# Performance work log

Measured on AMD Instinct MI355X. Metric: run time of the kernel, lower is better.

The kernel has to match this reference:

```python
import jax, jax.numpy as jnp
import numpy as np

N_NODES = 50000
N_EDGES = 800000
D_IN = 64
D_OUT = 64


def setup_inputs() -> dict:
    key = jax.random.key(0)
    k1, k2, k3, k4 = jax.random.split(key, 4)
    x = jax.random.normal(k1, (N_NODES, D_IN), dtype=jnp.float32)
    edge_index = jax.random.randint(k2, (2, N_EDGES), 0, N_NODES, dtype=jnp.int64)
    # GCNConv params: glorot weight [in, out], zero bias [out]
    limit = np.sqrt(6.0 / (D_IN + D_OUT)).astype(np.float32)
    W = jax.random.uniform(k3, (D_IN, D_OUT), minval=-limit, maxval=limit, dtype=jnp.float32)
    b = jnp.zeros((D_OUT,), dtype=jnp.float32)
    return {"x": x, "edge_index": edge_index, "W": W, "b": b}


def reference(x, edge_index, W, b):
    # GCNConv forward: linear transform, add self-loops, symmetric normalization,
    # scatter-add aggregation, bias.
    N = x.shape[0]
    xw = x @ W  # [N, D_OUT]

    self_loops = jnp.arange(N, dtype=edge_index.dtype)
    src = jnp.concatenate([edge_index[0], self_loops])  # source / neighbor j
    dst = jnp.concatenate([edge_index[1], self_loops])  # target / center i

    ones = jnp.ones_like(dst, dtype=xw.dtype)
    deg = jax.ops.segment_sum(ones, dst, num_segments=N)  # in-degree incl. self-loop
    deg_inv_sqrt = jnp.where(deg > 0, jax.lax.rsqrt(deg), 0.0)
    norm = deg_inv_sqrt[src] * deg_inv_sqrt[dst]  # [E+N]

    msgs = xw[src] * norm[:, None]  # gather + scale, [E+N, D_OUT]
    out = jax.ops.segment_sum(msgs, dst, num_segments=N)  # scatter-add
    return out + b
```

## Files before the change

kernel.cpp:

```cpp
#include <hip/hip_runtime.h>

constexpr int N_NODES = 50000;
constexpr int N_EDGES = 800000;
constexpr int D = 64;
constexpr int CAP = 64;
constexpr int NODES_PER_XCD = N_NODES / 8;

constexpr int OFF_CUR = 0;
constexpr int OFF_BKT = 50016;
constexpr int OFF_XW  = 3250016;

__device__ __forceinline__ float lo_bf(unsigned int u) {
    union { unsigned int x; float f; } c; c.x = u << 16; return c.f;
}
__device__ __forceinline__ float hi_bf(unsigned int u) {
    union { unsigned int x; float f; } c; c.x = u & 0xFFFF0000u; return c.f;
}
__device__ __forceinline__ unsigned short f2bf(float f) {
    union { float f; unsigned int u; } c; c.f = f;
    unsigned int r = (c.u + 0x7FFFu + ((c.u >> 16) & 1u)) >> 16;
    return (unsigned short)r;
}

__global__ void k_xw(const float* __restrict__ x, const float* __restrict__ W,
                     unsigned short* __restrict__ xw, int* __restrict__ cur) {
    int t = threadIdx.x;
    int zi = blockIdx.x * 256 + t;
    if (zi < N_NODES) cur[zi] = 0;
    __shared__ float sW[D * D];
    __shared__ float sx[4][D];
    for (int i = t; i < D * D; i += 256) sW[i] = W[i];
    int local = t >> 6;
    int j     = t & 63;
    int node  = blockIdx.x * 4 + local;
    sx[local][j] = (node < N_NODES) ? x[node * D + j] : 0.0f;
    __syncthreads();
    float acc = 0.0f;
    #pragma unroll
    for (int k = 0; k < D; ++k) acc += sx[local][k] * sW[k * D + j];
    if (node < N_NODES) xw[node * D + j] = f2bf(acc);
}

__global__ void k_place(const int4* __restrict__ src4, const int4* __restrict__ dst4,
                        int* __restrict__ cur, int* __restrict__ bucket) {
    int g   = blockIdx.x & 7;
    int bg  = blockIdx.x >> 3;
    int nbg = gridDim.x >> 3;
    int lo = g * NODES_PER_XCD, hi = lo + NODES_PER_XCD;
    int nq = N_EDGES / 4;
    for (int e = bg * blockDim.x + threadIdx.x; e < nq; e += nbg * blockDim.x) {
        int4 d = dst4[e];
        bool mx = (d.x >= lo) & (d.x < hi);
        bool my = (d.y >= lo) & (d.y < hi);
        bool mz = (d.z >= lo) & (d.z < hi);
        bool mw = (d.w >= lo) & (d.w < hi);
        if (mx | my | mz | mw) {
            int4 s = src4[e];
            if (mx) { int p = atomicAdd(&cur[d.x], 1); if (p < CAP) bucket[d.x * CAP + p] = s.x; }
            if (my) { int p = atomicAdd(&cur[d.y], 1); if (p < CAP) bucket[d.y * CAP + p] = s.y; }
            if (mz) { int p = atomicAdd(&cur[d.z], 1); if (p < CAP) bucket[d.z * CAP + p] = s.z; }
            if (mw) { int p = atomicAdd(&cur[d.w], 1); if (p < CAP) bucket[d.w * CAP + p] = s.w; }
        }
    }
}

__global__ void k_agg(const int* __restrict__ cur, const int* __restrict__ bucket,
                      const unsigned short* __restrict__ xw,
                      const float* __restrict__ b, float* __restrict__ out) {
    int t = threadIdx.x;
    int w = t >> 6, l = t & 63, g = l >> 3, q = l & 7;
    int i = blockIdx.x * 4 + w;
    if (i >= N_NODES) return;
    int deg = cur[i];
    float di = rsqrtf((float)(deg + 1));
    if (deg > CAP) deg = CAP;
    float a0 = 0.f, a1 = 0.f, a2 = 0.f, a3 = 0.f,
          a4 = 0.f, a5 = 0.f, a6 = 0.f, a7 = 0.f;
    const int* bkt = bucket + i * CAP;
    for (int k = g; k < deg; k += 8) {
        int s = bkt[k];
        float c = di * rsqrtf((float)(cur[s] + 1));
        uint4 v = *reinterpret_cast<const uint4*>(xw + s * D + q * 8);
        a0 += c * lo_bf(v.x); a1 += c * hi_bf(v.x);
        a2 += c * lo_bf(v.y); a3 += c * hi_bf(v.y);
        a4 += c * lo_bf(v.z); a5 += c * hi_bf(v.z);
        a6 += c * lo_bf(v.w); a7 += c * hi_bf(v.w);
    }
    a0 += __shfl_xor(a0, 8); a0 += __shfl_xor(a0, 16); a0 += __shfl_xor(a0, 32);
    a1 += __shfl_xor(a1, 8); a1 += __shfl_xor(a1, 16); a1 += __shfl_xor(a1, 32);
    a2 += __shfl_xor(a2, 8); a2 += __shfl_xor(a2, 16); a2 += __shfl_xor(a2, 32);
    a3 += __shfl_xor(a3, 8); a3 += __shfl_xor(a3, 16); a3 += __shfl_xor(a3, 32);
    a4 += __shfl_xor(a4, 8); a4 += __shfl_xor(a4, 16); a4 += __shfl_xor(a4, 32);
    a5 += __shfl_xor(a5, 8); a5 += __shfl_xor(a5, 16); a5 += __shfl_xor(a5, 32);
    a6 += __shfl_xor(a6, 8); a6 += __shfl_xor(a6, 16); a6 += __shfl_xor(a6, 32);
    a7 += __shfl_xor(a7, 8); a7 += __shfl_xor(a7, 16); a7 += __shfl_xor(a7, 32);
    if (g == 0) {
        uint4 sv = *reinterpret_cast<const uint4*>(xw + i * D + q * 8);
        float4 bv0 = *reinterpret_cast<const float4*>(b + q * 8);
        float4 bv1 = *reinterpret_cast<const float4*>(b + q * 8 + 4);
        float dd = di * di;
        float4 r0, r1;
        r0.x = a0 + dd * lo_bf(sv.x) + bv0.x;
        r0.y = a1 + dd * hi_bf(sv.x) + bv0.y;
        r0.z = a2 + dd * lo_bf(sv.y) + bv0.z;
        r0.w = a3 + dd * hi_bf(sv.y) + bv0.w;
        r1.x = a4 + dd * lo_bf(sv.z) + bv1.x;
        r1.y = a5 + dd * hi_bf(sv.z) + bv1.y;
        r1.z = a6 + dd * lo_bf(sv.w) + bv1.z;
        r1.w = a7 + dd * hi_bf(sv.w) + bv1.w;
        *reinterpret_cast<float4*>(out + i * D + q * 8)     = r0;
        *reinterpret_cast<float4*>(out + i * D + q * 8 + 4) = r1;
    }
}

extern "C" void kernel_launch(void* const* d_in, const int* in_sizes, int n_in,
                              void* d_out, int out_size, void* d_ws, size_t ws_size,
                              hipStream_t stream) {
    const float* x    = (const float*)d_in[0];
    const int*   edge = (const int*)d_in[1];
    const float* W    = (const float*)d_in[2];
    const float* b    = (const float*)d_in[3];
    float* out = (float*)d_out;

    const int4* src4 = (const int4*)edge;
    const int4* dst4 = (const int4*)(edge + N_EDGES);

    int* ws_i = (int*)d_ws;
    int* cur    = ws_i + OFF_CUR;
    int* bucket = ws_i + OFF_BKT;
    unsigned short* xw = (unsigned short*)(ws_i + OFF_XW);

    k_xw   <<<(N_NODES + 3) / 4, 256, 0, stream>>>(x, W, xw, cur);
    k_place<<<8 * 104, 256, 0, stream>>>(src4, dst4, cur, bucket);
    k_agg  <<<(N_NODES + 3) / 4, 256, 0, stream>>>(cur, bucket, xw, b, out);
}
```

Measured before the change: 158.3 us.

## Prescale transformed features by inverse sqrt degree and tile xw over 32 nodes

The linear-transform kernel now handles 32 nodes per block, so the 64x64 weight matrix is loaded into shared memory far fewer times. It writes fp32 results to a workspace buffer. A new scale kernel multiplies each row by its source node's inverse square-root degree, stores the result as bf16 and saves the per-node factor. Aggregation then sums prescaled neighbor rows and applies the destination factor once, removing the per-edge degree gather and rsqrt. The cost is an extra launch plus a round trip of the fp32 intermediate through memory.

```diff
diff --git a/kernel.cpp b/kernel.cpp
--- a/kernel.cpp
+++ b/kernel.cpp
@@ -5,10 +5,13 @@
 constexpr int D = 64;
 constexpr int CAP = 64;
 constexpr int NODES_PER_XCD = N_NODES / 8;
+constexpr int NPB = 32;
 
-constexpr int OFF_CUR = 0;
-constexpr int OFF_BKT = 50016;
-constexpr int OFF_XW  = 3250016;
+constexpr int OFF_CUR  = 0;
+constexpr int OFF_DISV = 50016;
+constexpr int OFF_BKT  = 100032;
+constexpr int OFF_XWF  = 3300032;
+constexpr int OFF_XW2  = 6500032;
 
 __device__ __forceinline__ float lo_bf(unsigned int u) {
     union { unsigned int x; float f; } c; c.x = u << 16; return c.f;
@@ -23,22 +26,35 @@
 }
 
 __global__ void k_xw(const float* __restrict__ x, const float* __restrict__ W,
-                     unsigned short* __restrict__ xw, int* __restrict__ cur) {
+                     float* __restrict__ xwf, int* __restrict__ cur) {
+    __shared__ float sW[D * D];
+    __shared__ float sx[NPB][D];
     int t = threadIdx.x;
     int zi = blockIdx.x * 256 + t;
     if (zi < N_NODES) cur[zi] = 0;
-    __shared__ float sW[D * D];
-    __shared__ float sx[4][D];
     for (int i = t; i < D * D; i += 256) sW[i] = W[i];
     int local = t >> 6;
     int j     = t & 63;
-    int node  = blockIdx.x * 4 + local;
-    sx[local][j] = (node < N_NODES) ? x[node * D + j] : 0.0f;
+    int base  = blockIdx.x * NPB;
+    #pragma unroll
+    for (int r = 0; r < NPB / 4; ++r) {
+        int node = base + r * 4 + local;
+        sx[r * 4 + local][j] = (node < N_NODES) ? x[node * D + j] : 0.0f;
+    }
     __syncthreads();
-    float acc = 0.0f;
+    float acc[NPB / 4];
     #pragma unroll
-    for (int k = 0; k < D; ++k) acc += sx[local][k] * sW[k * D + j];
-    if (node < N_NODES) xw[node * D + j] = f2bf(acc);
+    for (int r = 0; r < NPB / 4; ++r) acc[r] = 0.0f;
+    for (int k = 0; k < D; ++k) {
+        float wk = sW[k * D + j];
+        #pragma unroll
+        for (int r = 0; r < NPB / 4; ++r) acc[r] += sx[r * 4 + local][k] * wk;
+    }
+    #pragma unroll
+    for (int r = 0; r < NPB / 4; ++r) {
+        int node = base + r * 4 + local;
+        if (node < N_NODES) xwf[node * D + j] = acc[r];
+    }
 }
 
 __global__ void k_place(const int4* __restrict__ src4, const int4* __restrict__ dst4,
@@ -64,27 +80,41 @@
     }
 }
 
+__global__ void k_scale(const int* __restrict__ cur, const float4* __restrict__ xwf4,
+                        unsigned short* __restrict__ xw2, float* __restrict__ disv) {
+    int t = blockIdx.x * blockDim.x + threadIdx.x;
+    if (t >= N_NODES * D / 4) return;
+    int base = t * 4;
+    int i = base >> 6;
+    float dis = rsqrtf((float)(cur[i] + 1));
+    if ((base & 63) == 0) disv[i] = dis;
+    float4 v = xwf4[t];
+    ushort4 o;
+    o.x = f2bf(dis * v.x); o.y = f2bf(dis * v.y);
+    o.z = f2bf(dis * v.z); o.w = f2bf(dis * v.w);
+    *reinterpret_cast<ushort4*>(xw2 + base) = o;
+}
+
 __global__ void k_agg(const int* __restrict__ cur, const int* __restrict__ bucket,
-                      const unsigned short* __restrict__ xw,
+                      const unsigned short* __restrict__ xw2,
+                      const float* __restrict__ disv,
                       const float* __restrict__ b, float* __restrict__ out) {
     int t = threadIdx.x;
     int w = t >> 6, l = t & 63, g = l >> 3, q = l & 7;
     int i = blockIdx.x * 4 + w;
     if (i >= N_NODES) return;
     int deg = cur[i];
-    float di = rsqrtf((float)(deg + 1));
     if (deg > CAP) deg = CAP;
     float a0 = 0.f, a1 = 0.f, a2 = 0.f, a3 = 0.f,
           a4 = 0.f, a5 = 0.f, a6 = 0.f, a7 = 0.f;
     const int* bkt = bucket + i * CAP;
     for (int k = g; k < deg; k += 8) {
         int s = bkt[k];
-        float c = di * rsqrtf((float)(cur[s] + 1));
-        uint4 v = *reinterpret_cast<const uint4*>(xw + s * D + q * 8);
-        a0 += c * lo_bf(v.x); a1 += c * hi_bf(v.x);
-        a2 += c * lo_bf(v.y); a3 += c * hi_bf(v.y);
-        a4 += c * lo_bf(v.z); a5 += c * hi_bf(v.z);
-        a6 += c * lo_bf(v.w); a7 += c * hi_bf(v.w);
+        uint4 v = *reinterpret_cast<const uint4*>(xw2 + s * D + q * 8);
+        a0 += lo_bf(v.x); a1 += hi_bf(v.x);
+        a2 += lo_bf(v.y); a3 += hi_bf(v.y);
+        a4 += lo_bf(v.z); a5 += hi_bf(v.z);
+        a6 += lo_bf(v.w); a7 += hi_bf(v.w);
     }
     a0 += __shfl_xor(a0, 8); a0 += __shfl_xor(a0, 16); a0 += __shfl_xor(a0, 32);
     a1 += __shfl_xor(a1, 8); a1 += __shfl_xor(a1, 16); a1 += __shfl_xor(a1, 32);
@@ -95,19 +125,19 @@
     a6 += __shfl_xor(a6, 8); a6 += __shfl_xor(a6, 16); a6 += __shfl_xor(a6, 32);
     a7 += __shfl_xor(a7, 8); a7 += __shfl_xor(a7, 16); a7 += __shfl_xor(a7, 32);
     if (g == 0) {
-        uint4 sv = *reinterpret_cast<const uint4*>(xw + i * D + q * 8);
+        float di = disv[i];
+        uint4 sv = *reinterpret_cast<const uint4*>(xw2 + i * D + q * 8);
         float4 bv0 = *reinterpret_cast<const float4*>(b + q * 8);
         float4 bv1 = *reinterpret_cast<const float4*>(b + q * 8 + 4);
-        float dd = di * di;
         float4 r0, r1;
-        r0.x = a0 + dd * lo_bf(sv.x) + bv0.x;
-        r0.y = a1 + dd * hi_bf(sv.x) + bv0.y;
-        r0.z = a2 + dd * lo_bf(sv.y) + bv0.z;
-        r0.w = a3 + dd * hi_bf(sv.y) + bv0.w;
-        r1.x = a4 + dd * lo_bf(sv.z) + bv1.x;
-        r1.y = a5 + dd * hi_bf(sv.z) + bv1.y;
-        r1.z = a6 + dd * lo_bf(sv.w) + bv1.z;
-        r1.w = a7 + dd * hi_bf(sv.w) + bv1.w;
+        r0.x = di * (a0 + lo_bf(sv.x)) + bv0.x;
+        r0.y = di * (a1 + hi_bf(sv.x)) + bv0.y;
+        r0.z = di * (a2 + lo_bf(sv.y)) + bv0.z;
+        r0.w = di * (a3 + hi_bf(sv.y)) + bv0.w;
+        r1.x = di * (a4 + lo_bf(sv.z)) + bv1.x;
+        r1.y = di * (a5 + hi_bf(sv.z)) + bv1.y;
+        r1.z = di * (a6 + lo_bf(sv.w)) + bv1.z;
+        r1.w = di * (a7 + hi_bf(sv.w)) + bv1.w;
         *reinterpret_cast<float4*>(out + i * D + q * 8)     = r0;
         *reinterpret_cast<float4*>(out + i * D + q * 8 + 4) = r1;
     }
@@ -126,11 +156,14 @@
     const int4* dst4 = (const int4*)(edge + N_EDGES);
 
     int* ws_i = (int*)d_ws;
-    int* cur    = ws_i + OFF_CUR;
-    int* bucket = ws_i + OFF_BKT;
-    unsigned short* xw = (unsigned short*)(ws_i + OFF_XW);
+    int*   cur    = ws_i + OFF_CUR;
+    float* disv   = (float*)(ws_i + OFF_DISV);
+    int*   bucket = ws_i + OFF_BKT;
+    float* xwf    = (float*)(ws_i + OFF_XWF);
+    unsigned short* xw2 = (unsigned short*)(ws_i + OFF_XW2);
 
-    k_xw   <<<(N_NODES + 3) / 4, 256, 0, stream>>>(x, W, xw, cur);
+    k_xw   <<<(N_NODES + NPB - 1) / NPB, 256, 0, stream>>>(x, W, xwf, cur);
     k_place<<<8 * 104, 256, 0, stream>>>(src4, dst4, cur, bucket);
-    k_agg  <<<(N_NODES + 3) / 4, 256, 0, stream>>>(cur, bucket, xw, b, out);
+    k_scale<<<(N_NODES * D / 4 + 255) / 256, 256, 0, stream>>>(cur, (const float4*)xwf, xw2, disv);
+    k_agg  <<<(N_NODES + 3) / 4, 256, 0, stream>>>(cur, bucket, xw2, disv, b, out);
 }
```

Measured after the change: 156.9 us. Within noise of the previous version (-0.9%).
